# Optimization experiments

Hardware: AMD Instinct MI355X
Metric: run time of the kernel (lower is better)

The kernel has to match this reference:

```python
import jax, jax.numpy as jnp
import numpy as np

N = 50000          # nodes
E = 800000         # edges (avg degree 16)
NFEAT = 128        # dim_touched / gcn_nfeat
NHID = 96
NCLASS = 64
EXTRA = 32         # extra MLP-only features
NHID1, NHID2 = 128, 64
NN = 70            # top-k threshold rank
EPS = 1e-5         # BatchNorm1d eps


def setup_inputs() -> dict:
    key = jax.random.key(0)
    ks = jax.random.split(key, 24)
    x = jax.random.normal(ks[0], (N, NFEAT + EXTRA + 1), jnp.float32)
    grp = jax.random.randint(ks[1], (N,), 0, 2).astype(jnp.float32)
    x = x.at[:, -1].set(grp)  # last column is the group flag (target_group == 0)
    row = jax.random.randint(ks[2], (E,), 0, N, dtype=jnp.int32)
    col = jax.random.randint(ks[3], (E,), 0, N, dtype=jnp.int32)
    val = jax.random.uniform(ks[4], (E,), jnp.float32)

    def p(k, shape):
        return (jax.random.normal(k, shape, jnp.float32) * 0.05)

    return dict(
        x=x, row=row, col=col, val=val,
        W1=p(ks[5], (NFEAT, NHID)), b1=p(ks[6], (NHID,)),
        W2=p(ks[7], (NHID, NHID)), b2=p(ks[8], (NHID,)),
        W3=p(ks[9], (NHID, NHID)), b3=p(ks[10], (NHID,)),
        W4=p(ks[11], (NHID, NHID)), b4=p(ks[12], (NHID,)),
        W5=p(ks[13], (NHID, NCLASS)), b5=p(ks[14], (NCLASS,)),
        M1w=p(ks[15], (NCLASS + EXTRA, NHID1)), M1b=p(ks[16], (NHID1,)),
        M2w=p(ks[17], (NHID1, NHID2)), M2b=p(ks[18], (NHID2,)),
        M3w=p(ks[19], (NHID2, 1)), M3b=p(ks[20], (1,)),
    )


def _bn(h):
    # fresh BatchNorm1d in training mode, affine at default init (gamma=1, beta=0)
    m = jnp.mean(h, axis=0)
    v = jnp.mean((h - m) ** 2, axis=0)  # biased variance, as used for normalization
    return (h - m) * jax.lax.rsqrt(v + EPS)


def _gc(h, row, col, val, W, b):
    # GraphConvolution: spmm(adj, h @ W) + b, adj in COO form
    s = h @ W                                            # [N, out]
    msg = val[:, None] * s[col]                          # [E, out]
    agg = jax.ops.segment_sum(msg, row, num_segments=N)  # [N, out]
    return agg + b


def reference(x, row, col, val, W1, b1, W2, b2, W3, b3, W4, b4, W5, b5,
              M1w, M1b, M2w, M2b, M3w, M3b):
    h = x[:, :NFEAT]
    h = _bn(jax.nn.relu(_gc(h, row, col, val, W1, b1)))
    h = _bn(jax.nn.relu(_gc(h, row, col, val, W2, b2)))
    h = _bn(jax.nn.relu(_gc(h, row, col, val, W3, b3)))
    h = _bn(jax.nn.relu(_gc(h, row, col, val, W4, b4)))
    h = jax.nn.relu(_gc(h, row, col, val, W5, b5))        # [N, NCLASS]

    feat = jnp.concatenate([h, x[:, NFEAT:-1]], axis=1)   # [N, NCLASS+EXTRA]
    m = jax.nn.relu(feat @ M1w + M1b)
    m = jax.nn.relu(m @ M2w + M2b)
    m = m @ M3w + M3b                                     # [N, 1]

    # mask out target_group rows with the global min
    m = jnp.where(x[:, -1:] == 0.0, jnp.min(m), m)        # [N, 1]

    # top-70 threshold: value at descending rank NN
    thresh = jax.lax.top_k(m[:, 0], NN + 1)[0][NN]
    recip = jax.lax.stop_gradient(1.0 / m)                # torch reciprocal on detach()
    mask = jnp.where(m > thresh, recip, jnp.zeros_like(m))
    return m * mask
```

## Files before the change

### kernel.cpp

```cpp
#include <hip/hip_runtime.h>
#include <cstdint>
#include <cstddef>

#define XLD 161

typedef float f4u __attribute__((ext_vector_type(4), aligned(4)));
typedef float f4a __attribute__((ext_vector_type(4)));
typedef float f3u __attribute__((ext_vector_type(3), aligned(4)));

__global__ void hist_kernel(const int* __restrict__ row, int* __restrict__ cnt, int E) {
    for (int e = blockIdx.x * blockDim.x + threadIdx.x; e < E; e += gridDim.x * blockDim.x)
        atomicAdd(&cnt[row[e]], 1);
}

__global__ __launch_bounds__(256)
void scan1_kernel(const int* __restrict__ cnt, int* __restrict__ offs,
                  int* __restrict__ bsums, int n) {
    int t = threadIdx.x;
    int gid = blockIdx.x * 256 + t;
    int v = (gid < n) ? cnt[gid] : 0;
    int x = v;
#pragma unroll
    for (int o = 1; o < 64; o <<= 1) { int y = __shfl_up(x, o); if ((t & 63) >= o) x += y; }
    __shared__ int ws[4];
    if ((t & 63) == 63) ws[t >> 6] = x;
    __syncthreads();
    int add = 0;
    for (int w = 0; w < (t >> 6); w++) add += ws[w];
    int incl = x + add;
    if (gid < n) offs[gid] = incl - v;
    if (t == 255) bsums[blockIdx.x] = incl;
}

__global__ __launch_bounds__(256)
void scan2_kernel(int* __restrict__ bsums, int nb) {
    int t = threadIdx.x;
    int v = (t < nb) ? bsums[t] : 0;
    int x = v;
#pragma unroll
    for (int o = 1; o < 64; o <<= 1) { int y = __shfl_up(x, o); if ((t & 63) >= o) x += y; }
    __shared__ int ws[4];
    if ((t & 63) == 63) ws[t >> 6] = x;
    __syncthreads();
    int add = 0;
    for (int w = 0; w < (t >> 6); w++) add += ws[w];
    if (t < nb) bsums[t] = x + add - v;
}

__global__ void scan3_kernel(int* __restrict__ offs, int* __restrict__ cursor,
                             const int* __restrict__ bsums, int n, int E) {
    int gid = blockIdx.x * 256 + threadIdx.x;
    if (gid < n) {
        int o = offs[gid] + bsums[blockIdx.x];
        offs[gid] = o;
        cursor[gid] = o;
    }
    if (gid == 0) offs[n] = E;
}

__global__ void scatter_kernel(const int* __restrict__ row, const int* __restrict__ col,
                               const float* __restrict__ val, int* __restrict__ cursor,
                               int* __restrict__ colA, float* __restrict__ valA, int E) {
    for (int e = blockIdx.x * blockDim.x + threadIdx.x; e < E; e += gridDim.x * blockDim.x) {
        int r = row[e];
        int p = atomicAdd(&cursor[r], 1);
        colA[p] = col[e];
        valA[p] = val[e];
    }
}

template <int LC, bool WVS>
__global__ __launch_bounds__(256)
void aggP(const float* __restrict__ S, int ldS, const int* __restrict__ offs,
          const int* __restrict__ colA, const float* __restrict__ valA,
          float* __restrict__ Aout, float* __restrict__ vout, int n) {
    int lane = threadIdx.x & 63;
    int lg   = lane & 31;
    int grp  = threadIdx.x >> 5;
    int sh   = lane & 32;

    for (int node = blockIdx.x * 8 + grp; node < n; node += gridDim.x * 8) {
        int e0 = offs[node], e1 = offs[node + 1];
        float acc[LC];
#pragma unroll
        for (int a = 0; a < LC; a++) acc[a] = 0.f;
        float vsum = 0.f;

        for (int e = e0; e < e1; e += 32) {
            int   idx = e + lg;
            int   ce = (idx < e1) ? colA[idx] : 0;
            float ve = (idx < e1) ? valA[idx] : 0.f;
            int   cnt = min(32, e1 - e);
#pragma unroll 8
            for (int j = 0; j < cnt; j++) {
                int   c = __shfl(ce, sh + j);
                float v = __shfl(ve, sh + j);
                const float* srow = S + (size_t)c * ldS + LC * lg;
                if (LC == 3) {
                    f3u g = *(const f3u*)srow;
                    acc[0] = fmaf(v, g[0], acc[0]);
                    acc[1] = fmaf(v, g[1], acc[1]);
                    acc[2] = fmaf(v, g[2], acc[2]);
                } else {
                    f4u g = *(const f4u*)srow;
                    acc[0] = fmaf(v, g[0], acc[0]);
                    acc[1] = fmaf(v, g[1], acc[1]);
                    acc[2] = fmaf(v, g[2], acc[2]);
                    acc[3] = fmaf(v, g[3], acc[3]);
                }
                vsum += v;
            }
        }

        float* orow = Aout + (size_t)node * (32 * LC) + LC * lg;
        if (LC == 3) {
            f3u o; o[0] = acc[0]; o[1] = acc[1]; o[2] = acc[2];
            *(f3u*)orow = o;
        } else {
            f4u o; o[0] = acc[0]; o[1] = acc[1]; o[2] = acc[2]; o[3] = acc[3];
            *(f4u*)orow = o;
        }
        if (WVS && lg == 0) vout[node] = vsum;
    }
}

template <int CT>
__device__ inline void ldw(const float* p, float* wv) {
    if constexpr (CT == 4) { *(f4a*)wv = *(const f4a*)p; }
    else if constexpr (CT == 6) { *(f3u*)wv = *(const f3u*)p; *(f3u*)(wv + 3) = *(const f3u*)(p + 3); }
    else { *(f4a*)wv = *(const f4a*)p; *(f4a*)(wv + 4) = *(const f4a*)(p + 4); }
}

template <int K, int C, bool DOBN, bool HASCB>
__global__ __launch_bounds__(256)
void gemmF(const float* __restrict__ A1, int ld1, int split,
           const float* __restrict__ A2, int ld2,
           const float* __restrict__ W, const float* __restrict__ bias,
           const float* __restrict__ cbv, const float* __restrict__ vsum,
           float* __restrict__ Out, float* __restrict__ bsum,
           float* __restrict__ bsumsq, int n) {
    constexpr int CT = C / 16;
    __shared__ float Wc[16 * C];
    __shared__ float At[16][68];
    __shared__ float redS[DOBN ? C : 1];
    __shared__ float redQ[DOBN ? C : 1];

    int t  = threadIdx.x;
    int tc = t & 15, tr = t >> 4;
    int row0 = blockIdx.x * 64;

    if (DOBN && t < C) { redS[t] = 0.f; redQ[t] = 0.f; }

    int srow = t >> 2;
    int gr = row0 + srow; if (gr >= n) gr = n - 1;
    int kh = (t & 3) * 4;

    float acc[4][CT];
#pragma unroll
    for (int i = 0; i < 4; i++)
#pragma unroll
        for (int c = 0; c < CT; c++) acc[i][c] = 0.f;

    for (int kb = 0; kb < K; kb += 16) {
        __syncthreads();
        for (int i = t * 4; i < 16 * C; i += 1024)
            *(f4a*)&Wc[i] = *(const f4u*)&W[(size_t)kb * C + i];
        {
            int kg = kb + kh;
            const float* src = (kg < split) ? (A1 + (size_t)gr * ld1 + kg)
                                            : (A2 + (size_t)gr * ld2 + (kg - split));
            f4u v = *(const f4u*)src;
#pragma unroll
            for (int e = 0; e < 4; e++) At[kh + e][srow] = v[e];
        }
        __syncthreads();
#pragma unroll
        for (int kk = 0; kk < 16; kk++) {
            f4a av = *(const f4a*)&At[kk][tr * 4];
            float wv[CT];
            ldw<CT>(&Wc[kk * C + tc * CT], wv);
#pragma unroll
            for (int i = 0; i < 4; i++)
#pragma unroll
                for (int c = 0; c < CT; c++) acc[i][c] = fmaf(av[i], wv[c], acc[i][c]);
        }
    }

    float bb[CT], cc[CT];
#pragma unroll
    for (int c = 0; c < CT; c++) {
        bb[c] = bias[tc * CT + c];
        cc[c] = HASCB ? cbv[tc * CT + c] : 0.f;
    }
    float ps[CT], pq[CT];
#pragma unroll
    for (int c = 0; c < CT; c++) { ps[c] = 0.f; pq[c] = 0.f; }

#pragma unroll
    for (int i = 0; i < 4; i++) {
        int r = row0 + tr * 4 + i;
        if (r < n) {
            float vs = HASCB ? vsum[r] : 0.f;
            float* o = Out + (size_t)r * C + tc * CT;
#pragma unroll
            for (int c = 0; c < CT; c++) {
                float v = acc[i][c] + vs * cc[c] + bb[c];
                v = fmaxf(v, 0.f);
                o[c] = v;
                if (DOBN) { ps[c] += v; pq[c] += v * v; }
            }
        }
    }
    if (DOBN) {
#pragma unroll
        for (int c = 0; c < CT; c++) {
            ps[c] += __shfl_xor(ps[c], 16);
            ps[c] += __shfl_xor(ps[c], 32);
            pq[c] += __shfl_xor(pq[c], 16);
            pq[c] += __shfl_xor(pq[c], 32);
        }
        if ((t & 48) == 0) {
#pragma unroll
            for (int c = 0; c < CT; c++) {
                atomicAdd(&redS[tc * CT + c], ps[c]);
                atomicAdd(&redQ[tc * CT + c], pq[c]);
            }
        }
        __syncthreads();
        if (t < C) {
            atomicAdd(&bsum[t], redS[t]);
            atomicAdd(&bsumsq[t], redQ[t]);
        }
    }
}

template <int C>
__global__ __launch_bounds__(256)
void fold_kernel(const float* __restrict__ W, float* __restrict__ bsum,
                 float* __restrict__ bsumsq, float* __restrict__ Wf,
                 float* __restrict__ cb, int N) {
    __shared__ float mean[96], inv[96];
    int t = threadIdx.x;
    float rn = 1.0f / (float)N;
    if (t < 96) {
        float mu  = bsum[t] * rn;
        float var = bsumsq[t] * rn - mu * mu;
        mean[t] = mu;
        inv[t]  = rsqrtf(var + 1e-5f);
        bsum[t] = 0.f;
        bsumsq[t] = 0.f;
    }
    __syncthreads();
    for (int i = t; i < 96 * C; i += 256) {
        int k = i / C;
        Wf[i] = inv[k] * W[i];
    }
    if (t < C) {
        float s = 0.f;
        for (int k = 0; k < 96; k++) s += mean[k] * inv[k] * W[k * C + t];
        cb[t] = -s;
    }
}

__global__ __launch_bounds__(256)
void dot_min_kernel(const float* __restrict__ A, const float* __restrict__ M3w,
                    const float* __restrict__ M3b, float* __restrict__ m,
                    unsigned* __restrict__ gmin, int n) {
    int lane = threadIdx.x & 63;
    int wv   = threadIdx.x >> 6;
    float w  = M3w[lane];
    float b  = M3b[0];
    float lmin = 3.4e38f;
    int nw = gridDim.x * 4;
    for (int r = blockIdx.x * 4 + wv; r < n; r += nw) {
        float v = A[(size_t)r * 64 + lane] * w;
#pragma unroll
        for (int o = 32; o; o >>= 1) v += __shfl_down(v, o);
        if (lane == 0) {
            float mv = v + b;
            m[r] = mv;
            lmin = fminf(lmin, mv);
        }
    }
#pragma unroll
    for (int o = 32; o; o >>= 1) lmin = fminf(lmin, __shfl_down(lmin, o));
    __shared__ float sm[4];
    if (lane == 0) sm[wv] = lmin;
    __syncthreads();
    if (threadIdx.x == 0) {
        float mn = fminf(fminf(sm[0], sm[1]), fminf(sm[2], sm[3]));
        unsigned u = __float_as_uint(mn);
        unsigned key = (u >> 31) ? ~u : (u | 0x80000000u);
        atomicMin(gmin, key);
    }
}

__global__ void where_kernel(const float* __restrict__ x, float* __restrict__ m,
                             const unsigned* __restrict__ gmin, int n) {
    int i = blockIdx.x * blockDim.x + threadIdx.x;
    if (i < n) {
        unsigned k = *gmin;
        unsigned u = (k >> 31) ? (k ^ 0x80000000u) : ~k;
        float g = __uint_as_float(u);
        if (x[(size_t)i * XLD + 160] == 0.0f) m[i] = g;
    }
}

__device__ inline unsigned fkey(float f) {
    unsigned u = __float_as_uint(f);
    return (u >> 31) ? ~u : (u | 0x80000000u);
}

__global__ __launch_bounds__(1024)
void select_kernel(const float* __restrict__ m, int n, int kwant, float* __restrict__ thresh) {
    __shared__ unsigned hist[256];
    __shared__ unsigned sprefix;
    __shared__ int skk;
    int t = threadIdx.x;
    if (t == 0) { sprefix = 0u; skk = kwant; }
    for (int pass = 0; pass < 4; ++pass) {
        if (t < 256) hist[t] = 0u;
        __syncthreads();
        int shift = 24 - 8 * pass;
        unsigned pfx = sprefix;
        for (int i = t; i < n; i += 1024) {
            unsigned key = fkey(m[i]);
            bool ok = (pass == 0) || ((key >> (shift + 8)) == (pfx >> (shift + 8)));
            if (ok) atomicAdd(&hist[(key >> shift) & 255u], 1u);
        }
        __syncthreads();
        if (t == 0) {
            int cum = 0, kk = skk, chosen = 0;
            for (int b = 255; b >= 0; b--) {
                cum += (int)hist[b];
                if (cum >= kk) { chosen = b; kk -= (cum - (int)hist[b]); break; }
            }
            sprefix = pfx | ((unsigned)chosen << shift);
            skk = kk;
        }
        __syncthreads();
    }
    if (t == 0) {
        unsigned key = sprefix;
        unsigned u = (key >> 31) ? (key ^ 0x80000000u) : ~key;
        *thresh = __uint_as_float(u);
    }
}

__global__ void mask_kernel(const float* __restrict__ m, const float* __restrict__ thresh,
                            float* __restrict__ out, int n) {
    int i = blockIdx.x * blockDim.x + threadIdx.x;
    if (i < n) {
        float t = *thresh, v = m[i];
        out[i] = (v > t) ? v * (1.0f / v) : 0.0f;
    }
}

extern "C" void kernel_launch(void* const* d_in, const int* in_sizes, int n_in,
                              void* d_out, int out_size, void* d_ws, size_t ws_size,
                              hipStream_t stream) {
    const float* x   = (const float*)d_in[0];
    const int*   row = (const int*)d_in[1];
    const int*   col = (const int*)d_in[2];
    const float* val = (const float*)d_in[3];
    const float* W1  = (const float*)d_in[4];
    const float* b1  = (const float*)d_in[5];
    const float* W2  = (const float*)d_in[6];
    const float* b2  = (const float*)d_in[7];
    const float* W3  = (const float*)d_in[8];
    const float* b3  = (const float*)d_in[9];
    const float* W4  = (const float*)d_in[10];
    const float* b4  = (const float*)d_in[11];
    const float* W5  = (const float*)d_in[12];
    const float* b5  = (const float*)d_in[13];
    const float* M1w = (const float*)d_in[14];
    const float* M1b = (const float*)d_in[15];
    const float* M2w = (const float*)d_in[16];
    const float* M2b = (const float*)d_in[17];
    const float* M3w = (const float*)d_in[18];
    const float* M3b = (const float*)d_in[19];

    const int n = in_sizes[0] / XLD;
    const int E = in_sizes[1];

    char* ws = (char*)d_ws;
    size_t off = 0;
    auto carve = [&](size_t bytes) -> void* {
        void* p = ws + off;
        off = (off + bytes + 255) & ~(size_t)255;
        return p;
    };
    int*      offs   = (int*)carve((size_t)(n + 1) * 4);
    int*      cursor = (int*)carve((size_t)n * 4);
    int*      bsums  = (int*)carve(256 * 4);
    int*      colA   = (int*)carve((size_t)E * 4);
    float*    valA   = (float*)carve((size_t)E * 4);
    float*    h      = (float*)carve((size_t)n * 96 * 4);
    float*    big    = (float*)carve((size_t)n * 128 * 4);
    float*    Wf     = (float*)carve(96 * 96 * 4);
    float*    stats  = (float*)carve(192 * 4);
    float*    cb     = (float*)carve(96 * 4);
    float*    vsum   = (float*)carve((size_t)n * 4);
    float*    m      = (float*)carve((size_t)n * 4);
    unsigned* gmin   = (unsigned*)carve(4);
    float*    thresh = (float*)carve(4);
    float* bsum   = stats;
    float* bsumsq = stats + 96;

    hipMemsetAsync(cursor, 0, (size_t)n * 4, stream);
    hipMemsetAsync(stats, 0, 192 * 4, stream);
    hipMemsetAsync(gmin, 0xFF, 4, stream);

    const int nb = (n + 255) / 256;
    hist_kernel<<<512, 256, 0, stream>>>(row, cursor, E);
    scan1_kernel<<<nb, 256, 0, stream>>>(cursor, offs, bsums, n);
    scan2_kernel<<<1, 256, 0, stream>>>(bsums, nb);
    scan3_kernel<<<nb, 256, 0, stream>>>(offs, cursor, bsums, n, E);
    scatter_kernel<<<512, 256, 0, stream>>>(row, col, val, cursor, colA, valA, E);

    const int gB = (n + 63) / 64;
    const int ga = 3072;

    aggP<4, true><<<ga, 256, 0, stream>>>(x, XLD, offs, colA, valA, big, vsum, n);
    gemmF<128, 96, true, false><<<gB, 256, 0, stream>>>(big, 128, 128, big, 128,
        W1, b1, nullptr, nullptr, h, bsum, bsumsq, n);

    fold_kernel<96><<<1, 256, 0, stream>>>(W2, bsum, bsumsq, Wf, cb, n);
    aggP<3, false><<<ga, 256, 0, stream>>>(h, 96, offs, colA, valA, big, nullptr, n);
    gemmF<96, 96, true, true><<<gB, 256, 0, stream>>>(big, 96, 96, big, 96,
        Wf, b2, cb, vsum, h, bsum, bsumsq, n);

    fold_kernel<96><<<1, 256, 0, stream>>>(W3, bsum, bsumsq, Wf, cb, n);
    aggP<3, false><<<ga, 256, 0, stream>>>(h, 96, offs, colA, valA, big, nullptr, n);
    gemmF<96, 96, true, true><<<gB, 256, 0, stream>>>(big, 96, 96, big, 96,
        Wf, b3, cb, vsum, h, bsum, bsumsq, n);

    fold_kernel<96><<<1, 256, 0, stream>>>(W4, bsum, bsumsq, Wf, cb, n);
    aggP<3, false><<<ga, 256, 0, stream>>>(h, 96, offs, colA, valA, big, nullptr, n);
    gemmF<96, 96, true, true><<<gB, 256, 0, stream>>>(big, 96, 96, big, 96,
        Wf, b4, cb, vsum, h, bsum, bsumsq, n);

    fold_kernel<64><<<1, 256, 0, stream>>>(W5, bsum, bsumsq, Wf, cb, n);
    aggP<3, false><<<ga, 256, 0, stream>>>(h, 96, offs, colA, valA, big, nullptr, n);
    gemmF<96, 64, false, true><<<gB, 256, 0, stream>>>(big, 96, 96, big, 96,
        Wf, b5, cb, vsum, h, bsum, bsumsq, n);

    gemmF<96, 128, false, false><<<gB, 256, 0, stream>>>(h, 64, 64, x + 128, XLD,
        M1w, M1b, nullptr, nullptr, big, bsum, bsumsq, n);
    gemmF<128, 64, false, false><<<gB, 256, 0, stream>>>(big, 128, 128, big, 128,
        M2w, M2b, nullptr, nullptr, h, bsum, bsumsq, n);

    dot_min_kernel<<<256, 256, 0, stream>>>(h, M3w, M3b, m, gmin, n);

    where_kernel<<<(n + 255) / 256, 256, 0, stream>>>(x, m, gmin, n);

    select_kernel<<<1, 1024, 0, stream>>>(m, n, 71, thresh);

    mask_kernel<<<(n + 255) / 256, 256, 0, stream>>>(m, thresh, (float*)d_out, n);
}
```

Before: 819.3 us.

## Parallelize top-k threshold selection and interleave CSR column/value arrays

The single-block four-pass radix select over all N values is replaced by a multi-block 16-bit global histogram, a one-block prefix pick, a parallel collect of candidates that share the chosen prefix, and a small two-pass refinement over that candidate set. Separately, CSR column indices and edge values are packed into one int2 array, so each edge load in the aggregation kernels is a single 8-byte access instead of two 4-byte loads. The select change trades one serial kernel for four launches plus a 256KB histogram memset, and it relies on atomics into a global histogram that will contend when many keys share a bucket.

```diff
diff --git a/kernel.cpp b/kernel.cpp
--- a/kernel.cpp
+++ b/kernel.cpp
@@ -60,19 +60,18 @@
 
 __global__ void scatter_kernel(const int* __restrict__ row, const int* __restrict__ col,
                                const float* __restrict__ val, int* __restrict__ cursor,
-                               int* __restrict__ colA, float* __restrict__ valA, int E) {
+                               int2* __restrict__ cvA, int E) {
     for (int e = blockIdx.x * blockDim.x + threadIdx.x; e < E; e += gridDim.x * blockDim.x) {
         int r = row[e];
         int p = atomicAdd(&cursor[r], 1);
-        colA[p] = col[e];
-        valA[p] = val[e];
+        cvA[p] = make_int2(col[e], __float_as_int(val[e]));
     }
 }
 
 template <int LC, bool WVS>
 __global__ __launch_bounds__(256)
 void aggP(const float* __restrict__ S, int ldS, const int* __restrict__ offs,
-          const int* __restrict__ colA, const float* __restrict__ valA,
+          const int2* __restrict__ cvA,
           float* __restrict__ Aout, float* __restrict__ vout, int n) {
     int lane = threadIdx.x & 63;
     int lg   = lane & 31;
@@ -88,8 +87,9 @@
 
         for (int e = e0; e < e1; e += 32) {
             int   idx = e + lg;
-            int   ce = (idx < e1) ? colA[idx] : 0;
-            float ve = (idx < e1) ? valA[idx] : 0.f;
+            int2  cv = (idx < e1) ? cvA[idx] : make_int2(0, 0);
+            int   ce = cv.x;
+            float ve = __int_as_float(cv.y);
             int   cnt = min(32, e1 - e);
 #pragma unroll 8
             for (int j = 0; j < cnt; j++) {
@@ -311,22 +311,66 @@
     return (u >> 31) ? ~u : (u | 0x80000000u);
 }
 
+__global__ void sel_hist16(const float* __restrict__ m, unsigned* __restrict__ hist16, int n) {
+    for (int i = blockIdx.x * blockDim.x + threadIdx.x; i < n; i += gridDim.x * blockDim.x)
+        atomicAdd(&hist16[fkey(m[i]) >> 16], 1u);
+}
+
 __global__ __launch_bounds__(1024)
-void select_kernel(const float* __restrict__ m, int n, int kwant, float* __restrict__ thresh) {
+void sel_pick16(const unsigned* __restrict__ hist16, unsigned* __restrict__ pick, int k) {
+    int t = threadIdx.x;
+    int hi = 65535 - 64 * t;
+    unsigned s = 0;
+#pragma unroll 8
+    for (int j = 0; j < 64; j++) s += hist16[hi - j];
+    unsigned x = s;
+#pragma unroll
+    for (int o = 1; o < 64; o <<= 1) { unsigned y = __shfl_up(x, o); if ((t & 63) >= o) x += y; }
+    __shared__ unsigned ws[16];
+    if ((t & 63) == 63) ws[t >> 6] = x;
+    __syncthreads();
+    unsigned add = 0;
+    for (int w = 0; w < (t >> 6); w++) add += ws[w];
+    unsigned incl = x + add;
+    unsigned excl = incl - s;
+    if (excl < (unsigned)k && (unsigned)k <= incl) {
+        unsigned cum = excl;
+        for (int j = 0; j < 64; j++) {
+            unsigned c = hist16[hi - j];
+            if (cum + c >= (unsigned)k) { pick[0] = (unsigned)(hi - j); pick[1] = (unsigned)k - cum; break; }
+            cum += c;
+        }
+    }
+}
+
+__global__ void sel_collect(const float* __restrict__ m, const unsigned* __restrict__ pick,
+                            unsigned* __restrict__ sbuf, unsigned* __restrict__ scnt, int n) {
+    unsigned pfx = pick[0];
+    for (int i = blockIdx.x * blockDim.x + threadIdx.x; i < n; i += gridDim.x * blockDim.x) {
+        unsigned key = fkey(m[i]);
+        if ((key >> 16) == pfx) sbuf[atomicAdd(scnt, 1u)] = key;
+    }
+}
+
+__global__ __launch_bounds__(1024)
+void sel_final(const unsigned* __restrict__ sbuf, const unsigned* __restrict__ scnt,
+               const unsigned* __restrict__ pick, float* __restrict__ thresh) {
     __shared__ unsigned hist[256];
-    __shared__ unsigned sprefix;
+    __shared__ unsigned spfx;
     __shared__ int skk;
     int t = threadIdx.x;
-    if (t == 0) { sprefix = 0u; skk = kwant; }
-    for (int pass = 0; pass < 4; ++pass) {
+    int ns = (int)*scnt;
+    if (t == 0) { spfx = pick[0] << 16; skk = (int)pick[1]; }
+    __syncthreads();
+    for (int pass = 0; pass < 2; ++pass) {
         if (t < 256) hist[t] = 0u;
         __syncthreads();
-        int shift = 24 - 8 * pass;
-        unsigned pfx = sprefix;
-        for (int i = t; i < n; i += 1024) {
-            unsigned key = fkey(m[i]);
-            bool ok = (pass == 0) || ((key >> (shift + 8)) == (pfx >> (shift + 8)));
-            if (ok) atomicAdd(&hist[(key >> shift) & 255u], 1u);
+        int shift = 8 - 8 * pass;
+        unsigned pfxmask = (pass == 0) ? 0xFFFF0000u : 0xFFFFFF00u;
+        unsigned pfx = spfx;
+        for (int i = t; i < ns; i += 1024) {
+            unsigned key = sbuf[i];
+            if ((key & pfxmask) == pfx) atomicAdd(&hist[(key >> shift) & 255u], 1u);
         }
         __syncthreads();
         if (t == 0) {
@@ -335,13 +379,13 @@
                 cum += (int)hist[b];
                 if (cum >= kk) { chosen = b; kk -= (cum - (int)hist[b]); break; }
             }
-            sprefix = pfx | ((unsigned)chosen << shift);
+            spfx = pfx | ((unsigned)chosen << shift);
             skk = kk;
         }
         __syncthreads();
     }
     if (t == 0) {
-        unsigned key = sprefix;
+        unsigned key = spfx;
         unsigned u = (key >> 31) ? (key ^ 0x80000000u) : ~key;
         *thresh = __uint_as_float(u);
     }
@@ -393,8 +437,7 @@
     int*      offs   = (int*)carve((size_t)(n + 1) * 4);
     int*      cursor = (int*)carve((size_t)n * 4);
     int*      bsums  = (int*)carve(256 * 4);
-    int*      colA   = (int*)carve((size_t)E * 4);
-    float*    valA   = (float*)carve((size_t)E * 4);
+    int2*     cvA    = (int2*)carve((size_t)E * 8);
     float*    h      = (float*)carve((size_t)n * 96 * 4);
     float*    big    = (float*)carve((size_t)n * 128 * 4);
     float*    Wf     = (float*)carve(96 * 96 * 4);
@@ -404,44 +447,50 @@
     float*    m      = (float*)carve((size_t)n * 4);
     unsigned* gmin   = (unsigned*)carve(4);
     float*    thresh = (float*)carve(4);
+    unsigned* hist16 = (unsigned*)carve(65536 * 4);
+    unsigned* sbuf   = (unsigned*)carve((size_t)n * 4);
+    unsigned* scnt   = (unsigned*)carve(4);
+    unsigned* pick   = (unsigned*)carve(8);
     float* bsum   = stats;
     float* bsumsq = stats + 96;
 
     hipMemsetAsync(cursor, 0, (size_t)n * 4, stream);
     hipMemsetAsync(stats, 0, 192 * 4, stream);
     hipMemsetAsync(gmin, 0xFF, 4, stream);
+    hipMemsetAsync(hist16, 0, 65536 * 4, stream);
+    hipMemsetAsync(scnt, 0, 4, stream);
 
     const int nb = (n + 255) / 256;
     hist_kernel<<<512, 256, 0, stream>>>(row, cursor, E);
     scan1_kernel<<<nb, 256, 0, stream>>>(cursor, offs, bsums, n);
     scan2_kernel<<<1, 256, 0, stream>>>(bsums, nb);
     scan3_kernel<<<nb, 256, 0, stream>>>(offs, cursor, bsums, n, E);
-    scatter_kernel<<<512, 256, 0, stream>>>(row, col, val, cursor, colA, valA, E);
+    scatter_kernel<<<512, 256, 0, stream>>>(row, col, val, cursor, cvA, E);
 
     const int gB = (n + 63) / 64;
     const int ga = 3072;
 
-    aggP<4, true><<<ga, 256, 0, stream>>>(x, XLD, offs, colA, valA, big, vsum, n);
+    aggP<4, true><<<ga, 256, 0, stream>>>(x, XLD, offs, cvA, big, vsum, n);
     gemmF<128, 96, true, false><<<gB, 256, 0, stream>>>(big, 128, 128, big, 128,
         W1, b1, nullptr, nullptr, h, bsum, bsumsq, n);
 
     fold_kernel<96><<<1, 256, 0, stream>>>(W2, bsum, bsumsq, Wf, cb, n);
-    aggP<3, false><<<ga, 256, 0, stream>>>(h, 96, offs, colA, valA, big, nullptr, n);
+    aggP<3, false><<<ga, 256, 0, stream>>>(h, 96, offs, cvA, big, nullptr, n);
     gemmF<96, 96, true, true><<<gB, 256, 0, stream>>>(big, 96, 96, big, 96,
         Wf, b2, cb, vsum, h, bsum, bsumsq, n);
 
     fold_kernel<96><<<1, 256, 0, stream>>>(W3, bsum, bsumsq, Wf, cb, n);
-    aggP<3, false><<<ga, 256, 0, stream>>>(h, 96, offs, colA, valA, big, nullptr, n);
+    aggP<3, false><<<ga, 256, 0, stream>>>(h, 96, offs, cvA, big, nullptr, n);
     gemmF<96, 96, true, true><<<gB, 256, 0, stream>>>(big, 96, 96, big, 96,
         Wf, b3, cb, vsum, h, bsum, bsumsq, n);
 
     fold_kernel<96><<<1, 256, 0, stream>>>(W4, bsum, bsumsq, Wf, cb, n);
-    aggP<3, false><<<ga, 256, 0, stream>>>(h, 96, offs, colA, valA, big, nullptr, n);
+    aggP<3, false><<<ga, 256, 0, stream>>>(h, 96, offs, cvA, big, nullptr, n);
     gemmF<96, 96, true, true><<<gB, 256, 0, stream>>>(big, 96, 96, big, 96,
         Wf, b4, cb, vsum, h, bsum, bsumsq, n);
 
     fold_kernel<64><<<1, 256, 0, stream>>>(W5, bsum, bsumsq, Wf, cb, n);
-    aggP<3, false><<<ga, 256, 0, stream>>>(h, 96, offs, colA, valA, big, nullptr, n);
+    aggP<3, false><<<ga, 256, 0, stream>>>(h, 96, offs, cvA, big, nullptr, n);
     gemmF<96, 64, false, true><<<gB, 256, 0, stream>>>(big, 96, 96, big, 96,
         Wf, b5, cb, vsum, h, bsum, bsumsq, n);
 
@@ -454,7 +503,10 @@
 
     where_kernel<<<(n + 255) / 256, 256, 0, stream>>>(x, m, gmin, n);
 
-    select_kernel<<<1, 1024, 0, stream>>>(m, n, 71, thresh);
+    sel_hist16<<<256, 256, 0, stream>>>(m, hist16, n);
+    sel_pick16<<<1, 1024, 0, stream>>>(hist16, pick, 71);
+    sel_collect<<<256, 256, 0, stream>>>(m, pick, sbuf, scnt, n);
+    sel_final<<<1, 1024, 0, stream>>>(sbuf, scnt, pick, thresh);
 
     mask_kernel<<<(n + 255) / 256, 256, 0, stream>>>(m, thresh, (float*)d_out, n);
 }
```

Measured after the change: 1.071 ms. 1.31x slower.
